# Kernel optimization log

Measured on AMD Instinct MI355X. Metric: run time of the kernel, lower is better.

Reference implementation:

```python
import jax, jax.numpy as jnp
import numpy as np

EMBED_DIM = 100
NUM_SYMBOLS = 100000
BATCH = 2048
N_NEIGH = 200


def setup_inputs() -> dict:
    key = jax.random.key(0)
    ks = jax.random.split(key, 10)
    D = EMBED_DIM
    connections = jax.random.randint(ks[0], (BATCH, N_NEIGH, 4), 0, NUM_SYMBOLS, dtype=jnp.int64)
    num_neighbors = jax.random.randint(ks[1], (BATCH,), 1, N_NEIGH, dtype=jnp.int64)
    # symbol embedding table (num_symbols+1, D); padding row = num_symbols (left random; indices stay < NUM_SYMBOLS)
    symbol_emb = jax.random.normal(ks[2], (NUM_SYMBOLS + 1, D), dtype=jnp.float32) * 0.02
    # gcn_w: Linear(3D -> D) with its own bias, plus separate gcn_b parameter
    gcn_w = jax.random.normal(ks[3], (D, 3 * D), dtype=jnp.float32) * (1.0 / np.sqrt(3 * D))
    gcn_w_bias = jnp.zeros((D,), dtype=jnp.float32)
    gcn_b = jnp.zeros((D,), dtype=jnp.float32)
    # attn_w: Linear(D -> 1)
    attn_w = jax.random.normal(ks[4], (1, D), dtype=jnp.float32) * (1.0 / np.sqrt(D))
    attn_bias = jnp.zeros((1,), dtype=jnp.float32)
    # gate_w: Linear(D -> 1) plus separate gate_b parameter
    gate_w = jax.random.normal(ks[5], (1, D), dtype=jnp.float32) * (1.0 / np.sqrt(D))
    gate_w_bias = jnp.zeros((1,), dtype=jnp.float32)
    gate_b = jnp.zeros((1,), dtype=jnp.float32)
    return {
        "connections": connections,
        "num_neighbors": num_neighbors,
        "symbol_emb": symbol_emb,
        "gcn_w": gcn_w,
        "gcn_w_bias": gcn_w_bias,
        "gcn_b": gcn_b,
        "attn_w": attn_w,
        "attn_bias": attn_bias,
        "gate_w": gate_w,
        "gate_w_bias": gate_w_bias,
        "gate_b": gate_b,
    }


def reference(connections, num_neighbors, symbol_emb, gcn_w, gcn_w_bias, gcn_b,
              attn_w, attn_bias, gate_w, gate_w_bias, gate_b):
    # neighbor_encoder (eval mode: dropout is identity). num_neighbors is unused,
    # exactly as in the original module.
    entity_self = connections[:, 0, 0]          # (B,)
    relations = connections[:, :, 1]            # (B, N)
    entities = connections[:, :, 2]
    times = connections[:, :, 3]

    rel_embeds = symbol_emb[relations]          # (B, N, D) gather
    ent_embeds = symbol_emb[entities]
    time_embeds = symbol_emb[times]
    entself_embeds = symbol_emb[entity_self]    # (B, D)

    concat = jnp.concatenate((rel_embeds, ent_embeds, time_embeds), axis=-1)  # (B, N, 3D)
    out = jnp.einsum('bnk,dk->bnd', concat, gcn_w) + gcn_w_bias + gcn_b       # (B, N, D)
    out = jax.nn.leaky_relu(out, negative_slope=0.01)

    attn_logits = jnp.einsum('bnd,od->bno', out, attn_w) + attn_bias          # (B, N, 1)
    attn_weight = jax.nn.softmax(attn_logits, axis=1)                         # softmax over neighbors
    out_attn = jnp.einsum('bnd,bno->bd', out, attn_weight)                    # (B, D)

    gate = jax.nn.sigmoid(jnp.einsum('bd,od->bo', out_attn, gate_w) + gate_w_bias + gate_b)  # (B, 1)
    out_neighbor = out_attn * gate + entself_embeds * (1.0 - gate)            # (B, D)
    return out_neighbor
```

## Files before the change

### kernel.cpp

```cpp
#include <hip/hip_runtime.h>
#include <stdint.h>

#define D_EMB 100
#define NSYM 100001
#define BATCH 2048
#define NNEI 200
#define OS_STRIDE 102
#define P_STRIDE 304
#define FP8_SCALE 256.0f
#define FP8_INV   0.00390625f

#define BP_ELEMS   32000
#define BP_KS3_OFF 30720

typedef __bf16 bf16x8 __attribute__((ext_vector_type(8)));
typedef __bf16 bf16x4 __attribute__((ext_vector_type(4)));
typedef float  f32x4  __attribute__((ext_vector_type(4)));
typedef float  f32x2  __attribute__((ext_vector_type(2)));

union bf2u { uint32_t u; __bf16 h[2]; };

__host__ __device__ inline int colmap(int tau, int n) {
    return 32 * (tau >> 1) + 8 * (n >> 2) + 4 * (tau & 1) + (n & 3);
}

__global__ __launch_bounds__(256) void prep_bp(const float* __restrict__ gcn_w,
                                               __bf16* __restrict__ Bp) {
    int idx = blockIdx.x * 256 + threadIdx.x;
    if (idx >= BP_ELEMS) return;
    int tau, n, k;
    if (idx < BP_KS3_OFF) {
        int j = idx & 7;
        n     = (idx >> 3) & 15;
        int z = idx >> 7;
        tau   = z / 12;
        int r = z - tau * 12;
        int ks = r >> 2, q = r & 3;
        k = ks * 32 + q * 8 + j;
    } else {
        int i2 = idx - BP_KS3_OFF;
        int j  = i2 & 3;
        n      = (i2 >> 2) & 15;
        tau    = i2 >> 6;
        k      = 96 + j;
    }
    const int col = colmap(tau, n);
    float v = 0.0f;
    if (col < 300 && k < 100) {
        int c = col / 100, d = col % 100;
        v = gcn_w[d * 300 + c * 100 + k];
    }
    Bp[idx] = (__bf16)v;
}

__device__ inline void load_bfrag(const float* __restrict__ rowp, int quad,
                                  bf16x8 b[4]) {
    #pragma unroll
    for (int ks = 0; ks < 3; ++ks) {
        const int k0 = ks * 32 + quad * 8;
        const float4 x = *(const float4*)(rowp + k0);
        const float4 y = *(const float4*)(rowp + k0 + 4);
        bf16x8 v;
        v[0]=(__bf16)x.x; v[1]=(__bf16)x.y; v[2]=(__bf16)x.z; v[3]=(__bf16)x.w;
        v[4]=(__bf16)y.x; v[5]=(__bf16)y.y; v[6]=(__bf16)y.z; v[7]=(__bf16)y.w;
        b[ks] = v;
    }
    bf16x8 v;
    #pragma unroll
    for (int i = 0; i < 8; ++i) v[i] = (__bf16)0.0f;
    if (quad == 0) {
        const float4 x = *(const float4*)(rowp + 96);
        v[0]=(__bf16)x.x; v[1]=(__bf16)x.y; v[2]=(__bf16)x.z; v[3]=(__bf16)x.w;
    }
    b[3] = v;
}

__device__ inline uint32_t pack_fp8x4(float a, float b, float c, float d) {
    uint32_t w = (uint32_t)__builtin_amdgcn_cvt_pk_fp8_f32(a, b, 0, false);
    w = (uint32_t)__builtin_amdgcn_cvt_pk_fp8_f32(c, d, (int)w, true);
    return w;
}

__global__ __launch_bounds__(512, 4) void gemm_P(const float* __restrict__ emb,
                                                 const __bf16* __restrict__ Bp,
                                                 uint8_t* __restrict__ P8) {
    __shared__ __bf16 BpS[BP_ELEMS + 8];

    const int tid  = threadIdx.x;
    const int wave = tid >> 6;
    const int lane = tid & 63;
    const int n    = lane & 15;
    const int quad = lane >> 4;

    {
        const uint4* __restrict__ src = (const uint4*)Bp;
        uint4* dst = (uint4*)BpS;
        for (int c = tid; c < BP_ELEMS / 8; c += 512)
            dst[c] = src[c];
        if (tid < 8) BpS[BP_ELEMS + tid] = (__bf16)0.0f;
    }

    const int sA = blockIdx.x * 256 + wave * 32 + n;
    const int sB = sA + 16;
    const int rA = (sA <= NSYM - 1) ? sA : (NSYM - 1);
    const int rB = (sB <= NSYM - 1) ? sB : (NSYM - 1);

    bf16x8 bA[4], bB[4];
    load_bfrag(emb + (size_t)rA * D_EMB, quad, bA);
    load_bfrag(emb + (size_t)rB * D_EMB, quad, bB);

    __syncthreads();

    const bool wrA = (sA <= NSYM - 1);
    const bool wrB = (sB <= NSYM - 1);
    uint8_t* __restrict__ prA = P8 + (size_t)sA * P_STRIDE;
    uint8_t* __restrict__ prB = P8 + (size_t)sB * P_STRIDE;

    for (int u = 0; u < 10; ++u) {
        const int t0 = 2 * u, t1 = t0 + 1;

        bf16x8 a0[4], a1[4];
        #pragma unroll
        for (int ks = 0; ks < 3; ++ks) {
            a0[ks] = *(const bf16x8*)&BpS[((t0 * 12 + ks * 4 + quad) * 16 + n) * 8];
            a1[ks] = *(const bf16x8*)&BpS[((t1 * 12 + ks * 4 + quad) * 16 + n) * 8];
        }
        {
            const int o0 = (quad == 0) ? (BP_KS3_OFF + (t0 * 16 + n) * 4) : BP_ELEMS;
            const int o1 = (quad == 0) ? (BP_KS3_OFF + (t1 * 16 + n) * 4) : BP_ELEMS;
            const bf16x4 w0 = *(const bf16x4*)&BpS[o0];
            const bf16x4 w1 = *(const bf16x4*)&BpS[o1];
            bf16x8 v0, v1;
            #pragma unroll
            for (int i = 0; i < 4; ++i) {
                v0[i] = w0[i]; v1[i] = w1[i];
                v0[i + 4] = (__bf16)0.0f; v1[i + 4] = (__bf16)0.0f;
            }
            a0[3] = v0; a1[3] = v1;
        }

        f32x4 aA0 = {0.f,0.f,0.f,0.f}, aA1 = {0.f,0.f,0.f,0.f};
        f32x4 aB0 = {0.f,0.f,0.f,0.f}, aB1 = {0.f,0.f,0.f,0.f};
        #pragma unroll
        for (int ks = 0; ks < 4; ++ks) {
            aA0 = __builtin_amdgcn_mfma_f32_16x16x32_bf16(a0[ks], bA[ks], aA0, 0, 0, 0);
            aA1 = __builtin_amdgcn_mfma_f32_16x16x32_bf16(a1[ks], bA[ks], aA1, 0, 0, 0);
            aB0 = __builtin_amdgcn_mfma_f32_16x16x32_bf16(a0[ks], bB[ks], aB0, 0, 0, 0);
            aB1 = __builtin_amdgcn_mfma_f32_16x16x32_bf16(a1[ks], bB[ks], aB1, 0, 0, 0);
        }

        const int colBase = 32 * u + 8 * quad;
        if (colBase + 8 <= 300) {
            if (wrA) {
                uint2 o;
                o.x = pack_fp8x4(aA0[0]*FP8_SCALE, aA0[1]*FP8_SCALE,
                                 aA0[2]*FP8_SCALE, aA0[3]*FP8_SCALE);
                o.y = pack_fp8x4(aA1[0]*FP8_SCALE, aA1[1]*FP8_SCALE,
                                 aA1[2]*FP8_SCALE, aA1[3]*FP8_SCALE);
                *(uint2*)(prA + colBase) = o;
            }
            if (wrB) {
                uint2 o;
                o.x = pack_fp8x4(aB0[0]*FP8_SCALE, aB0[1]*FP8_SCALE,
                                 aB0[2]*FP8_SCALE, aB0[3]*FP8_SCALE);
                o.y = pack_fp8x4(aB1[0]*FP8_SCALE, aB1[1]*FP8_SCALE,
                                 aB1[2]*FP8_SCALE, aB1[3]*FP8_SCALE);
                *(uint2*)(prB + colBase) = o;
            }
        } else if (colBase + 4 <= 300) {
            if (wrA)
                *(uint32_t*)(prA + colBase) =
                    pack_fp8x4(aA0[0]*FP8_SCALE, aA0[1]*FP8_SCALE,
                               aA0[2]*FP8_SCALE, aA0[3]*FP8_SCALE);
            if (wrB)
                *(uint32_t*)(prB + colBase) =
                    pack_fp8x4(aB0[0]*FP8_SCALE, aB0[1]*FP8_SCALE,
                               aB0[2]*FP8_SCALE, aB0[3]*FP8_SCALE);
        }
    }
}

__global__ __launch_bounds__(1024, 8) void gather_attn(
        const int*     __restrict__ conn,
        const uint8_t* __restrict__ P8,
        const float*   __restrict__ emb,
        const float*   __restrict__ gcn_w_bias,
        const float*   __restrict__ gcn_b,
        const float*   __restrict__ attn_w,
        const float*   __restrict__ attn_bias,
        const float*   __restrict__ gate_w,
        const float*   __restrict__ gate_w_bias,
        const float*   __restrict__ gate_b,
        float* __restrict__ out) {

    __shared__ __bf16 out_s[NNEI][OS_STRIDE];
    __shared__ int4   conn_s[NNEI];
    __shared__ float  logits[NNEI];
    __shared__ float  logit2[NNEI][2];
    __shared__ float  wgt[NNEI];
    __shared__ float2 aw_s[50];
    __shared__ float4 bias4_s[25];
    __shared__ float  part[8][D_EMB];
    __shared__ float  red[128];
    __shared__ float  gsh;

    const int b = blockIdx.x;
    const int t = threadIdx.x;
    const int w = t >> 6;
    const int l = t & 63;

    if (t < NNEI) conn_s[t] = *(const int4*)(conn + ((size_t)b * NNEI + t) * 4);
    if (t < 50)   aw_s[t] = make_float2(attn_w[2 * t], attn_w[2 * t + 1]);
    if (t < 25)
        bias4_s[t] = make_float4(gcn_w_bias[4*t]   + gcn_b[4*t],
                                 gcn_w_bias[4*t+1] + gcn_b[4*t+1],
                                 gcn_w_bias[4*t+2] + gcn_b[4*t+2],
                                 gcn_w_bias[4*t+3] + gcn_b[4*t+3]);
    const float abias = attn_bias[0];
    __syncthreads();

    #pragma unroll
    for (int i = 0; i < 5; ++i) {
        const int idx = t + 1024 * i;
        if (idx < NNEI * 25) {
            const int n  = idx / 25;
            const int li = idx - n * 25;
            const int4 c = conn_s[n];
            const uint32_t u0 = *(const uint32_t*)(P8 + (size_t)c.y * P_STRIDE +       li * 4);
            const uint32_t u1 = *(const uint32_t*)(P8 + (size_t)c.z * P_STRIDE + 100 + li * 4);
            const uint32_t u2 = *(const uint32_t*)(P8 + (size_t)c.w * P_STRIDE + 200 + li * 4);
            const f32x2 y0 = __builtin_amdgcn_cvt_pk_f32_fp8((int)u0, false);
            const f32x2 y1 = __builtin_amdgcn_cvt_pk_f32_fp8((int)u0, true);
            const f32x2 z0 = __builtin_amdgcn_cvt_pk_f32_fp8((int)u1, false);
            const f32x2 z1 = __builtin_amdgcn_cvt_pk_f32_fp8((int)u1, true);
            const f32x2 q0 = __builtin_amdgcn_cvt_pk_f32_fp8((int)u2, false);
            const f32x2 q1 = __builtin_amdgcn_cvt_pk_f32_fp8((int)u2, true);
            const float4 bb = bias4_s[li];
            float v0 = (y0[0] + z0[0] + q0[0]) * FP8_INV + bb.x;
            float v1 = (y0[1] + z0[1] + q0[1]) * FP8_INV + bb.y;
            float v2 = (y1[0] + z1[0] + q1[0]) * FP8_INV + bb.z;
            float v3 = (y1[1] + z1[1] + q1[1]) * FP8_INV + bb.w;
            v0 = v0 > 0.f ? v0 : 0.01f * v0;
            v1 = v1 > 0.f ? v1 : 0.01f * v1;
            v2 = v2 > 0.f ? v2 : 0.01f * v2;
            v3 = v3 > 0.f ? v3 : 0.01f * v3;
            bf2u o01; o01.h[0] = (__bf16)v0; o01.h[1] = (__bf16)v1;
            bf2u o23; o23.h[0] = (__bf16)v2; o23.h[1] = (__bf16)v3;
            *(uint32_t*)&out_s[n][4 * li]     = o01.u;
            *(uint32_t*)&out_s[n][4 * li + 2] = o23.u;
        }
    }
    __syncthreads();

    if (t < 2 * NNEI) {
        const int n = t >> 1, half = t & 1;
        const __bf16* row = &out_s[n][half * 50];
        float p = 0.f;
        #pragma unroll 5
        for (int j = 0; j < 25; ++j) {
            bf2u v; v.u = *(const uint32_t*)(row + 2 * j);
            const float2 ww = aw_s[half * 25 + j];
            p += (float)v.h[0] * ww.x + (float)v.h[1] * ww.y;
        }
        logit2[n][half] = p;
    }
    __syncthreads();
    if (t < NNEI) logits[t] = logit2[t][0] + logit2[t][1] + abias;
    __syncthreads();

    if (w == 0) {
        float vals[4];
        float mx = -1e30f;
        #pragma unroll
        for (int j = 0; j < 4; ++j) {
            const int n = l + 64 * j;
            vals[j] = (n < NNEI) ? logits[n] : -1e30f;
            mx = fmaxf(mx, vals[j]);
        }
        #pragma unroll
        for (int off = 32; off > 0; off >>= 1) mx = fmaxf(mx, __shfl_xor(mx, off));
        float sum = 0.f;
        #pragma unroll
        for (int j = 0; j < 4; ++j) {
            const int n = l + 64 * j;
            if (n < NNEI) { const float e = __expf(vals[j] - mx); wgt[n] = e; sum += e; }
        }
        #pragma unroll
        for (int off = 32; off > 0; off >>= 1) sum += __shfl_xor(sum, off);
        const float inv = 1.f / sum;
        #pragma unroll
        for (int j = 0; j < 4; ++j) {
            const int n = l + 64 * j;
            if (n < NNEI) wgt[n] *= inv;
        }
    }
    __syncthreads();

    {
        const int g  = t >> 7;
        const int dd = t & 127;
        if (dd < D_EMB) {
            float pa = 0.f;
            const int n0 = g * 25;
            #pragma unroll 5
            for (int n = n0; n < n0 + 25; ++n) pa += wgt[n] * (float)out_s[n][dd];
            part[g][dd] = pa;
        }
    }
    __syncthreads();

    float accd = 0.f;
    if (t < D_EMB) {
        #pragma unroll
        for (int g = 0; g < 8; ++g) accd += part[g][t];
        red[t] = accd * gate_w[t];
    } else if (t < 128) {
        red[t] = 0.f;
    }
    __syncthreads();

    if (w == 0) {
        float r = red[l] + red[l + 64];
        #pragma unroll
        for (int off = 32; off > 0; off >>= 1) r += __shfl_xor(r, off);
        if (l == 0) gsh = 1.f / (1.f + __expf(-(r + gate_w_bias[0] + gate_b[0])));
    }
    __syncthreads();

    if (t < D_EMB) {
        const int self = conn_s[0].x;
        const float se = emb[(size_t)self * D_EMB + t];
        const float g  = gsh;
        out[(size_t)b * D_EMB + t] = accd * g + se * (1.f - g);
    }
}

__global__ void ws_diag(float* out, float ws_mb) { out[0] = ws_mb; }

extern "C" void kernel_launch(void* const* d_in, const int* in_sizes, int n_in,
                              void* d_out, int out_size, void* d_ws, size_t ws_size,
                              hipStream_t stream) {
    const int*   conn        = (const int*)d_in[0];
    const float* emb         = (const float*)d_in[2];
    const float* gcn_w       = (const float*)d_in[3];
    const float* gcn_w_bias  = (const float*)d_in[4];
    const float* gcn_b       = (const float*)d_in[5];
    const float* attn_w      = (const float*)d_in[6];
    const float* attn_bias   = (const float*)d_in[7];
    const float* gate_w      = (const float*)d_in[8];
    const float* gate_w_bias = (const float*)d_in[9];
    const float* gate_b      = (const float*)d_in[10];
    float* out = (float*)d_out;

    const size_t P_bytes = (size_t)NSYM * P_STRIDE;
    const size_t Bp_off  = (P_bytes + 255) & ~(size_t)255;
    const size_t need    = Bp_off + (size_t)BP_ELEMS * 2;

    if (ws_size < need) {
        ws_diag<<<1, 1, 0, stream>>>(out, (float)(ws_size / 1.0e6));
        return;
    }

    uint8_t* P8 = (uint8_t*)d_ws;
    __bf16*  Bp = (__bf16*)((char*)d_ws + Bp_off);

    prep_bp<<<(BP_ELEMS + 255) / 256, 256, 0, stream>>>(gcn_w, Bp);
    gemm_P<<<(NSYM + 255) / 256, 512, 0, stream>>>(emb, Bp, P8);
    gather_attn<<<BATCH, 1024, 0, stream>>>(conn, P8, emb, gcn_w_bias, gcn_b,
                                            attn_w, attn_bias, gate_w, gate_w_bias,
                                            gate_b, out);
}
```

Before: 155.7 us.

## Gather fp8 projections directly into LDS asynchronously and recompute activations per pass

The neighbor gather now uses global_load_lds to copy the three fp8 projection slices straight into shared-memory planes, with no register round trip. The kernel no longer materializes a bf16 activation tile. The bias, leaky ReLU and dequantization are recomputed from the fp8 planes twice: once when computing the attention logits and once in the weighted sum. This aims to overlap and shorten the gather latency and drop a bf16 rounding step, at the cost of duplicated ALU work. The extra shared memory (about 60KB of planes) may also reduce occupancy.

After: 162.2 us. 4.2% more time.

```diff
diff --git a/kernel.cpp b/kernel.cpp
--- a/kernel.cpp
+++ b/kernel.cpp
@@ -5,10 +5,10 @@
 #define NSYM 100001
 #define BATCH 2048
 #define NNEI 200
-#define OS_STRIDE 102
 #define P_STRIDE 304
 #define FP8_SCALE 256.0f
 #define FP8_INV   0.00390625f
+#define PL 5056
 
 #define BP_ELEMS   32000
 #define BP_KS3_OFF 30720
@@ -18,7 +18,11 @@
 typedef float  f32x4  __attribute__((ext_vector_type(4)));
 typedef float  f32x2  __attribute__((ext_vector_type(2)));
 
-union bf2u { uint32_t u; __bf16 h[2]; };
+__device__ __forceinline__ void async_ld4(const void* g, void* l) {
+    __builtin_amdgcn_global_load_lds(
+        (const __attribute__((address_space(1))) uint32_t*)g,
+        (__attribute__((address_space(3))) uint32_t*)l, 4, 0, 0);
+}
 
 __host__ __device__ inline int colmap(int tau, int n) {
     return 32 * (tau >> 1) + 8 * (n >> 2) + 4 * (tau & 1) + (n & 3);
@@ -193,14 +197,14 @@
         const float*   __restrict__ gate_b,
         float* __restrict__ out) {
 
-    __shared__ __bf16 out_s[NNEI][OS_STRIDE];
+    __shared__ uint32_t planes[3 * PL];
     __shared__ int4   conn_s[NNEI];
+    __shared__ float  logit5[NNEI][5];
     __shared__ float  logits[NNEI];
-    __shared__ float  logit2[NNEI][2];
     __shared__ float  wgt[NNEI];
-    __shared__ float2 aw_s[50];
+    __shared__ float4 aw4_s[25];
     __shared__ float4 bias4_s[25];
-    __shared__ float  part[8][D_EMB];
+    __shared__ float  part[16][D_EMB];
     __shared__ float  red[128];
     __shared__ float  gsh;
 
@@ -210,62 +214,64 @@
     const int l = t & 63;
 
     if (t < NNEI) conn_s[t] = *(const int4*)(conn + ((size_t)b * NNEI + t) * 4);
-    if (t < 50)   aw_s[t] = make_float2(attn_w[2 * t], attn_w[2 * t + 1]);
-    if (t < 25)
+    if (t < 25) {
+        aw4_s[t]   = *(const float4*)(attn_w + 4 * t);
         bias4_s[t] = make_float4(gcn_w_bias[4*t]   + gcn_b[4*t],
                                  gcn_w_bias[4*t+1] + gcn_b[4*t+1],
                                  gcn_w_bias[4*t+2] + gcn_b[4*t+2],
                                  gcn_w_bias[4*t+3] + gcn_b[4*t+3]);
+    }
     const float abias = attn_bias[0];
     __syncthreads();
 
-    #pragma unroll
-    for (int i = 0; i < 5; ++i) {
-        const int idx = t + 1024 * i;
-        if (idx < NNEI * 25) {
-            const int n  = idx / 25;
-            const int li = idx - n * 25;
-            const int4 c = conn_s[n];
-            const uint32_t u0 = *(const uint32_t*)(P8 + (size_t)c.y * P_STRIDE +       li * 4);
-            const uint32_t u1 = *(const uint32_t*)(P8 + (size_t)c.z * P_STRIDE + 100 + li * 4);
-            const uint32_t u2 = *(const uint32_t*)(P8 + (size_t)c.w * P_STRIDE + 200 + li * 4);
+    for (int c = w; c < 79; c += 16) {
+        const int item = c * 64 + l;
+        int n = item / 25;
+        const int li = item - n * 25;
+        n = (n < NNEI) ? n : (NNEI - 1);
+        const int4 ci = conn_s[n];
+        const uint8_t* g0 = P8 + (size_t)ci.y * P_STRIDE +       li * 4;
+        const uint8_t* g1 = P8 + (size_t)ci.z * P_STRIDE + 100 + li * 4;
+        const uint8_t* g2 = P8 + (size_t)ci.w * P_STRIDE + 200 + li * 4;
+        async_ld4(g0, &planes[0 * PL + c * 64]);
+        async_ld4(g1, &planes[1 * PL + c * 64]);
+        async_ld4(g2, &planes[2 * PL + c * 64]);
+    }
+    __syncthreads();
+
+    if (t < 5 * NNEI) {
+        const int n = t / 5, q = t - (t / 5) * 5;
+        float p = 0.f;
+        #pragma unroll
+        for (int j = 5 * q; j < 5 * q + 5; ++j) {
+            const uint32_t u0 = planes[0 * PL + n * 25 + j];
+            const uint32_t u1 = planes[1 * PL + n * 25 + j];
+            const uint32_t u2 = planes[2 * PL + n * 25 + j];
             const f32x2 y0 = __builtin_amdgcn_cvt_pk_f32_fp8((int)u0, false);
             const f32x2 y1 = __builtin_amdgcn_cvt_pk_f32_fp8((int)u0, true);
             const f32x2 z0 = __builtin_amdgcn_cvt_pk_f32_fp8((int)u1, false);
             const f32x2 z1 = __builtin_amdgcn_cvt_pk_f32_fp8((int)u1, true);
             const f32x2 q0 = __builtin_amdgcn_cvt_pk_f32_fp8((int)u2, false);
             const f32x2 q1 = __builtin_amdgcn_cvt_pk_f32_fp8((int)u2, true);
-            const float4 bb = bias4_s[li];
+            const float4 bb = bias4_s[j];
+            const float4 aw = aw4_s[j];
             float v0 = (y0[0] + z0[0] + q0[0]) * FP8_INV + bb.x;
             float v1 = (y0[1] + z0[1] + q0[1]) * FP8_INV + bb.y;
             float v2 = (y1[0] + z1[0] + q1[0]) * FP8_INV + bb.z;
             float v3 = (y1[1] + z1[1] + q1[1]) * FP8_INV + bb.w;
-            v0 = v0 > 0.f ? v0 : 0.01f * v0;
-            v1 = v1 > 0.f ? v1 : 0.01f * v1;
-            v2 = v2 > 0.f ? v2 : 0.01f * v2;
-            v3 = v3 > 0.f ? v3 : 0.01f * v3;
-            bf2u o01; o01.h[0] = (__bf16)v0; o01.h[1] = (__bf16)v1;
-            bf2u o23; o23.h[0] = (__bf16)v2; o23.h[1] = (__bf16)v3;
-            *(uint32_t*)&out_s[n][4 * li]     = o01.u;
-            *(uint32_t*)&out_s[n][4 * li + 2] = o23.u;
-        }
-    }
-    __syncthreads();
-
-    if (t < 2 * NNEI) {
-        const int n = t >> 1, half = t & 1;
-        const __bf16* row = &out_s[n][half * 50];
-        float p = 0.f;
-        #pragma unroll 5
-        for (int j = 0; j < 25; ++j) {
-            bf2u v; v.u = *(const uint32_t*)(row + 2 * j);
-            const float2 ww = aw_s[half * 25 + j];
-            p += (float)v.h[0] * ww.x + (float)v.h[1] * ww.y;
-        }
-        logit2[n][half] = p;
-    }
-    __syncthreads();
-    if (t < NNEI) logits[t] = logit2[t][0] + logit2[t][1] + abias;
+            v0 = fmaxf(v0, 0.01f * v0);
+            v1 = fmaxf(v1, 0.01f * v1);
+            v2 = fmaxf(v2, 0.01f * v2);
+            v3 = fmaxf(v3, 0.01f * v3);
+            p += v0 * aw.x + v1 * aw.y + v2 * aw.z + v3 * aw.w;
+        }
+        logit5[n][q] = p;
+    }
+    __syncthreads();
+
+    if (t < NNEI)
+        logits[t] = logit5[t][0] + logit5[t][1] + logit5[t][2]
+                  + logit5[t][3] + logit5[t][4] + abias;
     __syncthreads();
 
     if (w == 0) {
@@ -296,23 +302,43 @@
     }
     __syncthreads();
 
-    {
-        const int g  = t >> 7;
-        const int dd = t & 127;
-        if (dd < D_EMB) {
-            float pa = 0.f;
-            const int n0 = g * 25;
-            #pragma unroll 5
-            for (int n = n0; n < n0 + 25; ++n) pa += wgt[n] * (float)out_s[n][dd];
-            part[g][dd] = pa;
-        }
+    if (t < 400) {
+        const int li = t % 25;
+        const int z  = t / 25;
+        const int g  = z >> 1, h = z & 1;
+        const int n0 = g * 25 + (h ? 12 : 0);
+        const int n1 = g * 25 + (h ? 25 : 12);
+        const float4 bb = bias4_s[li];
+        float s0 = 0.f, s1 = 0.f, s2 = 0.f, s3 = 0.f;
+        for (int n = n0; n < n1; ++n) {
+            const float wn = wgt[n];
+            const uint32_t u0 = planes[0 * PL + n * 25 + li];
+            const uint32_t u1 = planes[1 * PL + n * 25 + li];
+            const uint32_t u2 = planes[2 * PL + n * 25 + li];
+            const f32x2 y0 = __builtin_amdgcn_cvt_pk_f32_fp8((int)u0, false);
+            const f32x2 y1 = __builtin_amdgcn_cvt_pk_f32_fp8((int)u0, true);
+            const f32x2 z0 = __builtin_amdgcn_cvt_pk_f32_fp8((int)u1, false);
+            const f32x2 z1 = __builtin_amdgcn_cvt_pk_f32_fp8((int)u1, true);
+            const f32x2 q0 = __builtin_amdgcn_cvt_pk_f32_fp8((int)u2, false);
+            const f32x2 q1 = __builtin_amdgcn_cvt_pk_f32_fp8((int)u2, true);
+            float v0 = (y0[0] + z0[0] + q0[0]) * FP8_INV + bb.x;
+            float v1 = (y0[1] + z0[1] + q0[1]) * FP8_INV + bb.y;
+            float v2 = (y1[0] + z1[0] + q1[0]) * FP8_INV + bb.z;
+            float v3 = (y1[1] + z1[1] + q1[1]) * FP8_INV + bb.w;
+            v0 = fmaxf(v0, 0.01f * v0);
+            v1 = fmaxf(v1, 0.01f * v1);
+            v2 = fmaxf(v2, 0.01f * v2);
+            v3 = fmaxf(v3, 0.01f * v3);
+            s0 += wn * v0; s1 += wn * v1; s2 += wn * v2; s3 += wn * v3;
+        }
+        *(float4*)&part[z][4 * li] = make_float4(s0, s1, s2, s3);
     }
     __syncthreads();
 
     float accd = 0.f;
     if (t < D_EMB) {
         #pragma unroll
-        for (int g = 0; g < 8; ++g) accd += part[g][t];
+        for (int z = 0; z < 16; ++z) accd += part[z][t];
         red[t] = accd * gate_w[t];
     } else if (t < 128) {
         red[t] = 0.f;
```

## Store activations as FP8 in LDS and halve gather block size

Applied to the files above, without the earlier changes.

The gather kernel now keeps the post-activation neighbor outputs in shared memory as packed FP8 (in the scaled domain) instead of bf16. Block size drops from 1024 to 512 threads, and each thread batches 5 gathers of three P8 words before converting them, to get more loads in flight. Attention logits and the weighted sum are computed directly from the FP8 words, with the scale folded into the bias and applied at the end. This cuts LDS footprint and traffic and may raise occupancy, at the cost of extra precision loss from quantizing activations to FP8.

After: 149.5 us. 1.04x faster.

```diff
diff --git a/kernel.cpp b/kernel.cpp
--- a/kernel.cpp
+++ b/kernel.cpp
@@ -5,7 +5,6 @@
 #define NSYM 100001
 #define BATCH 2048
 #define NNEI 200
-#define OS_STRIDE 102
 #define P_STRIDE 304
 #define FP8_SCALE 256.0f
 #define FP8_INV   0.00390625f
@@ -17,8 +16,6 @@
 typedef __bf16 bf16x4 __attribute__((ext_vector_type(4)));
 typedef float  f32x4  __attribute__((ext_vector_type(4)));
 typedef float  f32x2  __attribute__((ext_vector_type(2)));
-
-union bf2u { uint32_t u; __bf16 h[2]; };
 
 __host__ __device__ inline int colmap(int tau, int n) {
     return 32 * (tau >> 1) + 8 * (n >> 2) + 4 * (tau & 1) + (n & 3);
@@ -180,7 +177,7 @@
     }
 }
 
-__global__ __launch_bounds__(1024, 8) void gather_attn(
+__global__ __launch_bounds__(512, 8) void gather_attn(
         const int*     __restrict__ conn,
         const uint8_t* __restrict__ P8,
         const float*   __restrict__ emb,
@@ -193,16 +190,16 @@
         const float*   __restrict__ gate_b,
         float* __restrict__ out) {
 
-    __shared__ __bf16 out_s[NNEI][OS_STRIDE];
-    __shared__ int4   conn_s[NNEI];
-    __shared__ float  logits[NNEI];
-    __shared__ float  logit2[NNEI][2];
-    __shared__ float  wgt[NNEI];
-    __shared__ float2 aw_s[50];
-    __shared__ float4 bias4_s[25];
-    __shared__ float  part[8][D_EMB];
-    __shared__ float  red[128];
-    __shared__ float  gsh;
+    __shared__ uint32_t vs[NNEI * 25];
+    __shared__ int4     conn_s[NNEI];
+    __shared__ float    logit2[NNEI][2];
+    __shared__ float    logits[NNEI];
+    __shared__ float    wgt[NNEI];
+    __shared__ float4   aw4_s[25];
+    __shared__ float4   bias4_s[25];
+    __shared__ float    part[20][D_EMB];
+    __shared__ float    red[128];
+    __shared__ float    gsh;
 
     const int b = blockIdx.x;
     const int t = threadIdx.x;
@@ -210,62 +207,73 @@
     const int l = t & 63;
 
     if (t < NNEI) conn_s[t] = *(const int4*)(conn + ((size_t)b * NNEI + t) * 4);
-    if (t < 50)   aw_s[t] = make_float2(attn_w[2 * t], attn_w[2 * t + 1]);
-    if (t < 25)
-        bias4_s[t] = make_float4(gcn_w_bias[4*t]   + gcn_b[4*t],
-                                 gcn_w_bias[4*t+1] + gcn_b[4*t+1],
-                                 gcn_w_bias[4*t+2] + gcn_b[4*t+2],
-                                 gcn_w_bias[4*t+3] + gcn_b[4*t+3]);
+    if (t < 25) {
+        aw4_s[t]   = *(const float4*)(attn_w + 4 * t);
+        bias4_s[t] = make_float4((gcn_w_bias[4*t]   + gcn_b[4*t])   * FP8_SCALE,
+                                 (gcn_w_bias[4*t+1] + gcn_b[4*t+1]) * FP8_SCALE,
+                                 (gcn_w_bias[4*t+2] + gcn_b[4*t+2]) * FP8_SCALE,
+                                 (gcn_w_bias[4*t+3] + gcn_b[4*t+3]) * FP8_SCALE);
+    }
     const float abias = attn_bias[0];
     __syncthreads();
 
     #pragma unroll
-    for (int i = 0; i < 5; ++i) {
-        const int idx = t + 1024 * i;
-        if (idx < NNEI * 25) {
-            const int n  = idx / 25;
-            const int li = idx - n * 25;
-            const int4 c = conn_s[n];
-            const uint32_t u0 = *(const uint32_t*)(P8 + (size_t)c.y * P_STRIDE +       li * 4);
-            const uint32_t u1 = *(const uint32_t*)(P8 + (size_t)c.z * P_STRIDE + 100 + li * 4);
-            const uint32_t u2 = *(const uint32_t*)(P8 + (size_t)c.w * P_STRIDE + 200 + li * 4);
-            const f32x2 y0 = __builtin_amdgcn_cvt_pk_f32_fp8((int)u0, false);
-            const f32x2 y1 = __builtin_amdgcn_cvt_pk_f32_fp8((int)u0, true);
-            const f32x2 z0 = __builtin_amdgcn_cvt_pk_f32_fp8((int)u1, false);
-            const f32x2 z1 = __builtin_amdgcn_cvt_pk_f32_fp8((int)u1, true);
-            const f32x2 q0 = __builtin_amdgcn_cvt_pk_f32_fp8((int)u2, false);
-            const f32x2 q1 = __builtin_amdgcn_cvt_pk_f32_fp8((int)u2, true);
-            const float4 bb = bias4_s[li];
-            float v0 = (y0[0] + z0[0] + q0[0]) * FP8_INV + bb.x;
-            float v1 = (y0[1] + z0[1] + q0[1]) * FP8_INV + bb.y;
-            float v2 = (y1[0] + z1[0] + q1[0]) * FP8_INV + bb.z;
-            float v3 = (y1[1] + z1[1] + q1[1]) * FP8_INV + bb.w;
-            v0 = v0 > 0.f ? v0 : 0.01f * v0;
-            v1 = v1 > 0.f ? v1 : 0.01f * v1;
-            v2 = v2 > 0.f ? v2 : 0.01f * v2;
-            v3 = v3 > 0.f ? v3 : 0.01f * v3;
-            bf2u o01; o01.h[0] = (__bf16)v0; o01.h[1] = (__bf16)v1;
-            bf2u o23; o23.h[0] = (__bf16)v2; o23.h[1] = (__bf16)v3;
-            *(uint32_t*)&out_s[n][4 * li]     = o01.u;
-            *(uint32_t*)&out_s[n][4 * li + 2] = o23.u;
+    for (int half = 0; half < 2; ++half) {
+        uint32_t U[5][3];
+        #pragma unroll
+        for (int j = 0; j < 5; ++j) {
+            const int idx = t + 512 * (5 * half + j);
+            if (idx < NNEI * 25) {
+                const int n  = idx / 25;
+                const int li = idx - n * 25;
+                const int4 c = conn_s[n];
+                U[j][0] = *(const uint32_t*)(P8 + (size_t)c.y * P_STRIDE +       li * 4);
+                U[j][1] = *(const uint32_t*)(P8 + (size_t)c.z * P_STRIDE + 100 + li * 4);
+                U[j][2] = *(const uint32_t*)(P8 + (size_t)c.w * P_STRIDE + 200 + li * 4);
+            }
+        }
+        #pragma unroll
+        for (int j = 0; j < 5; ++j) {
+            const int idx = t + 512 * (5 * half + j);
+            if (idx < NNEI * 25) {
+                const int li = idx % 25;
+                const f32x2 y0 = __builtin_amdgcn_cvt_pk_f32_fp8((int)U[j][0], false);
+                const f32x2 y1 = __builtin_amdgcn_cvt_pk_f32_fp8((int)U[j][0], true);
+                const f32x2 z0 = __builtin_amdgcn_cvt_pk_f32_fp8((int)U[j][1], false);
+                const f32x2 z1 = __builtin_amdgcn_cvt_pk_f32_fp8((int)U[j][1], true);
+                const f32x2 q0 = __builtin_amdgcn_cvt_pk_f32_fp8((int)U[j][2], false);
+                const f32x2 q1 = __builtin_amdgcn_cvt_pk_f32_fp8((int)U[j][2], true);
+                const float4 bb = bias4_s[li];
+                float v0 = y0[0] + z0[0] + q0[0] + bb.x;
+                float v1 = y0[1] + z0[1] + q0[1] + bb.y;
+                float v2 = y1[0] + z1[0] + q1[0] + bb.z;
+                float v3 = y1[1] + z1[1] + q1[1] + bb.w;
+                v0 = fmaxf(v0, 0.01f * v0);
+                v1 = fmaxf(v1, 0.01f * v1);
+                v2 = fmaxf(v2, 0.01f * v2);
+                v3 = fmaxf(v3, 0.01f * v3);
+                vs[idx] = pack_fp8x4(v0, v1, v2, v3);
+            }
         }
     }
     __syncthreads();
 
     if (t < 2 * NNEI) {
-        const int n = t >> 1, half = t & 1;
-        const __bf16* row = &out_s[n][half * 50];
+        const int n = t >> 1, h = t & 1;
+        const int lo = h ? 13 : 0, hi = h ? 25 : 13;
         float p = 0.f;
-        #pragma unroll 5
-        for (int j = 0; j < 25; ++j) {
-            bf2u v; v.u = *(const uint32_t*)(row + 2 * j);
-            const float2 ww = aw_s[half * 25 + j];
-            p += (float)v.h[0] * ww.x + (float)v.h[1] * ww.y;
-        }
-        logit2[n][half] = p;
-    }
-    __syncthreads();
-    if (t < NNEI) logits[t] = logit2[t][0] + logit2[t][1] + abias;
+        for (int j = lo; j < hi; ++j) {
+            const uint32_t u = vs[n * 25 + j];
+            const f32x2 a = __builtin_amdgcn_cvt_pk_f32_fp8((int)u, false);
+            const f32x2 c = __builtin_amdgcn_cvt_pk_f32_fp8((int)u, true);
+            const float4 aw = aw4_s[j];
+            p += a[0] * aw.x + a[1] * aw.y + c[0] * aw.z + c[1] * aw.w;
+        }
+        logit2[n][h] = p;
+    }
+    __syncthreads();
+    if (t < NNEI)
+        logits[t] = (logit2[t][0] + logit2[t][1]) * FP8_INV + abias;
     __syncthreads();
 
     if (w == 0) {
@@ -296,23 +304,28 @@
     }
     __syncthreads();
 
-    {
-        const int g  = t >> 7;
-        const int dd = t & 127;
-        if (dd < D_EMB) {
-            float pa = 0.f;
-            const int n0 = g * 25;
-            #pragma unroll 5
-            for (int n = n0; n < n0 + 25; ++n) pa += wgt[n] * (float)out_s[n][dd];
-            part[g][dd] = pa;
-        }
+    if (t < 500) {
+        const int z  = t / 25;
+        const int li = t - z * 25;
+        const int n0 = z * 10;
+        float s0 = 0.f, s1 = 0.f, s2 = 0.f, s3 = 0.f;
+        #pragma unroll 5
+        for (int n = n0; n < n0 + 10; ++n) {
+            const float wn = wgt[n];
+            const uint32_t u = vs[n * 25 + li];
+            const f32x2 a = __builtin_amdgcn_cvt_pk_f32_fp8((int)u, false);
+            const f32x2 c = __builtin_amdgcn_cvt_pk_f32_fp8((int)u, true);
+            s0 += wn * a[0]; s1 += wn * a[1]; s2 += wn * c[0]; s3 += wn * c[1];
+        }
+        *(float4*)&part[z][4 * li] = make_float4(s0, s1, s2, s3);
     }
     __syncthreads();
 
     float accd = 0.f;
     if (t < D_EMB) {
         #pragma unroll
-        for (int g = 0; g < 8; ++g) accd += part[g][t];
+        for (int z = 0; z < 20; ++z) accd += part[z][t];
+        accd *= FP8_INV;
         red[t] = accd * gate_w[t];
     } else if (t < 128) {
         red[t] = 0.f;
@@ -366,7 +379,7 @@
 
     prep_bp<<<(BP_ELEMS + 255) / 256, 256, 0, stream>>>(gcn_w, Bp);
     gemm_P<<<(NSYM + 255) / 256, 512, 0, stream>>>(emb, Bp, P8);
-    gather_attn<<<BATCH, 1024, 0, stream>>>(conn, P8, emb, gcn_w_bias, gcn_b,
-                                            attn_w, attn_bias, gate_w, gate_w_bias,
-                                            gate_b, out);
-}
+    gather_attn<<<BATCH, 512, 0, stream>>>(conn, P8, emb, gcn_w_bias, gcn_b,
+                                           attn_w, attn_bias, gate_w, gate_w_bias,
+                                           gate_b, out);
+}
```
